# Kernel optimization log

Measured on AMD Instinct MI355X. Metric: run time of the kernel, lower is better.

## Reference

```python
import jax, jax.numpy as jnp
import numpy as np

N_NODES = 50000
N_EDGES = 500000
MUL0, MUL1 = 16, 8          # multiplicities of 0e and 1o irreps (in == out)
DIM = MUL0 + 3 * MUL1       # 40
N_BASIS, MID = 10, 32
WNUM = MUL0*MUL0 + MUL1*MUL0 + MUL0*MUL1 + MUL1*MUL1  # 576
INV_SQRT3 = 1.0 / np.sqrt(3.0)  # wigner-3j normalization for l=1 paths
FAN_IN = MUL0 + MUL1        # paths into each output irrep: 16 + 8 = 24
A0 = np.sqrt(1.0 / FAN_IN)  # sqrt((2*0+1)/fan_in)
A1 = np.sqrt(3.0 / FAN_IN)  # sqrt((2*1+1)/fan_in)
LN_EPS = 1e-5


def setup_inputs() -> dict:
    key = jax.random.key(0)
    ks = jax.random.split(key, 8)
    return {
        "x": jax.random.normal(ks[0], (N_NODES, DIM), jnp.float32),
        "edge_sh": jax.random.normal(ks[1], (N_EDGES, 4), jnp.float32),
        "edge_length_embedded": jax.random.uniform(ks[2], (N_EDGES, N_BASIS), jnp.float32),
        "W1": jax.random.normal(ks[3], (N_BASIS, MID), jnp.float32),
        "W2": jax.random.normal(ks[4], (MID, WNUM), jnp.float32),
        "gamma": jnp.ones((DIM,), jnp.float32),
        "beta": jnp.zeros((DIM,), jnp.float32),
        "edge_src": jax.random.randint(ks[5], (N_EDGES,), 0, N_NODES),
        "edge_dst": jax.random.randint(ks[6], (N_EDGES,), 0, N_NODES),
        "avg_num_neighbors": 10,
    }


def reference(x, edge_sh, edge_length_embedded, W1, W2, gamma, beta,
              edge_src, edge_dst, avg_num_neighbors):
    # radial MLP -> per-edge tensor-product weights (e3nn FullyConnectedNet style)
    h = jax.nn.silu(edge_length_embedded @ W1 / jnp.sqrt(jnp.float32(N_BASIS)))
    w = h @ W2 / jnp.sqrt(jnp.float32(MID))              # [E, 576]

    # gather node features onto edges and split into irrep blocks
    xg = x[edge_src]                                     # [E, 40]
    s = xg[:, :MUL0]                                     # [E, 16]  scalars 0e
    v = xg[:, MUL0:].reshape(-1, MUL1, 3)                # [E, 8, 3] vectors 1o
    sh0 = edge_sh[:, 0]                                  # [E]
    sh1 = edge_sh[:, 1:4]                                # [E, 3]

    # split per-edge weights by tensor-product path
    o0, o1, o2 = MUL0*MUL0, MUL0*MUL0 + MUL1*MUL0, MUL0*MUL0 + MUL1*MUL0 + MUL0*MUL1
    W_ss0 = w[:, :o0].reshape(-1, MUL0, MUL0)            # 0e x 0e -> 0e
    W_vv0 = w[:, o0:o1].reshape(-1, MUL1, MUL0)          # 1o x 1o -> 0e
    W_sv1 = w[:, o1:o2].reshape(-1, MUL0, MUL1)          # 0e x 1o -> 1o
    W_vs1 = w[:, o2:].reshape(-1, MUL1, MUL1)            # 1o x 0e -> 1o

    # weighted Clebsch-Gordan tensor product (per edge)
    vdot = jnp.einsum('eui,ei->eu', v, sh1) * INV_SQRT3  # CG 1x1->0
    out0 = A0 * (jnp.einsum('euk,eu->ek', W_ss0, s * sh0[:, None])
                 + jnp.einsum('euk,eu->ek', W_vv0, vdot))            # [E, 16]
    out1 = A1 * INV_SQRT3 * (
        jnp.einsum('euk,eu->ek', W_sv1, s)[:, :, None] * sh1[:, None, :]
        + jnp.einsum('euk,eui->eki', W_vs1, v) * sh0[:, None, None])  # [E, 8, 3]
    edge_values = jnp.concatenate([out0, out1.reshape(-1, 3 * MUL1)], axis=1)

    # scatter-sum into destination nodes, degree normalization, layernorm
    node = jax.ops.segment_sum(edge_values, edge_dst, num_segments=N_NODES)
    node = node / jnp.sqrt(jnp.float32(avg_num_neighbors))
    mu = node.mean(axis=-1, keepdims=True)
    var = node.var(axis=-1, keepdims=True)
    return (node - mu) * jax.lax.rsqrt(var + LN_EPS) * gamma + beta
```

## Files before the change

### kernel.cpp

```cpp
#include <hip/hip_runtime.h>
#include <hip/hip_bf16.h>

#define N_NODES 50000
#define N_EDGES 500000
#define MUL0 16
#define MUL1 8
#define DIM 40
#define N_BASIS 10
#define MID 32
#define WNUM 576
#define SCAN_BLOCKS 196
#define N_GROUPS (N_EDGES / 16)

typedef __attribute__((ext_vector_type(8))) short bf16x8_t;
typedef __attribute__((ext_vector_type(4))) float f32x4_t;

__device__ __forceinline__ float bf2f(unsigned short u) {
  return __uint_as_float(((unsigned int)u) << 16);
}
__device__ __forceinline__ unsigned short f2bf(float f) {
  unsigned int x = __float_as_uint(f);
  unsigned int r = x + 0x7fffu + ((x >> 16) & 1u);
  return (unsigned short)(r >> 16);
}
__device__ __forceinline__ unsigned pk2bf(float a, float b) {
  float2 f; f.x = a; f.y = b;
  __hip_bfloat162 h = __float22bfloat162_rn(f);
  return *reinterpret_cast<unsigned*>(&h);
}
__device__ __forceinline__ bool detect_bf16(const void* gamma) {
  return ((const unsigned int*)gamma)[0] == 0x3F803F80u;
}
template <bool BF16>
__device__ __forceinline__ float ld(const void* p, size_t i) {
  if (BF16) return bf2f(((const unsigned short*)p)[i]);
  return ((const float*)p)[i];
}

#define C_INV_SQRT10 0.31622776601683794f
#define C_INV_SQRT32 0.17677669529663687f
#define C_INV_SQRT3  0.5773502691896258f
#define C_A0C        0.20412414523193154f

__device__ __forceinline__ f32x4_t mfma16x16x32(bf16x8_t a, bf16x8_t b, f32x4_t c) {
  return __builtin_amdgcn_mfma_f32_16x16x32_bf16(a, b, c, 0, 0, 0);
}

__global__ __launch_bounds__(256) void rank_kernel(
    const int* __restrict__ edge_dst, int* __restrict__ cnt,
    int* __restrict__ rank) {
  int e = blockIdx.x * 256 + threadIdx.x;
  if (e < N_EDGES) rank[e] = atomicAdd(&cnt[edge_dst[e]], 1);
}

__global__ __launch_bounds__(256) void scanA_kernel(
    const int* __restrict__ cnt, int* __restrict__ off, int* __restrict__ btot) {
  __shared__ int s[256];
  const int tid = threadIdx.x;
  const int i = blockIdx.x * 256 + tid;
  int v = (i < N_NODES) ? cnt[i] : 0;
  s[tid] = v;
  __syncthreads();
  for (int d = 1; d < 256; d <<= 1) {
    int t = (tid >= d) ? s[tid - d] : 0;
    __syncthreads();
    s[tid] += t;
    __syncthreads();
  }
  if (i < N_NODES) off[i] = s[tid] - v;
  if (tid == 255) btot[blockIdx.x] = s[255];
}

__global__ __launch_bounds__(256) void scanB_kernel(
    const int* __restrict__ btot, int* __restrict__ bbase) {
  __shared__ int s[256];
  const int tid = threadIdx.x;
  int v = (tid < SCAN_BLOCKS) ? btot[tid] : 0;
  s[tid] = v;
  __syncthreads();
  for (int d = 1; d < 256; d <<= 1) {
    int t = (tid >= d) ? s[tid - d] : 0;
    __syncthreads();
    s[tid] += t;
    __syncthreads();
  }
  if (tid < SCAN_BLOCKS) bbase[tid] = s[tid] - v;
}


template <bool BF16>
__device__ void edge_mfma_body(
    const void* __restrict__ x,
    const void* __restrict__ edge_sh,
    const void* __restrict__ elemb,
    const void* __restrict__ W1,
    const void* __restrict__ W2,
    const int* __restrict__ edge_src,
    const int* __restrict__ edge_dst,
    const int* __restrict__ rank,
    const int* __restrict__ off,
    const int* __restrict__ bbase,
    unsigned short* __restrict__ ev,
    short* __restrict__ w2b, float* __restrict__ w1s, float* __restrict__ stg)
{
  const int tid = threadIdx.x;

  for (int i = tid; i < 36 * 512; i += 256) {
    int m = i / WNUM;
    int col = i - m * WNUM;
    int q = m >> 3, j = m & 7;
    int t = col >> 4, n = col & 15;
    short val;
    if (BF16) val = (short)((const unsigned short*)W2)[i];
    else      val = (short)f2bf(((const float*)W2)[i]);
    w2b[t * 512 + q * 128 + n * 8 + j] = val;
  }
  for (int i = tid; i < N_BASIS * MID; i += 256) w1s[i] = ld<BF16>(W1, i);
  __syncthreads();

  const int lane = tid & 63;
  const int wid  = tid >> 6;
  const int quad = lane >> 4;
  const int l16  = lane & 15;
  float* S = stg + wid * 832;

  for (int gi = blockIdx.x * 4 + wid; gi < N_GROUPS; gi += gridDim.x * 4) {
    const int e0 = gi * 16;
    __builtin_amdgcn_wave_barrier();

    const int eL   = e0 + l16;
    const int dL   = edge_dst[eL];
    const int posv = off[dL] + bbase[dL >> 8] + rank[eL];
    const int posA = __shfl(posv, lane >> 2, 64);
    const int posB = posv;

    if (lane < 16) {
      if (BF16) {
        uint2 sw = *reinterpret_cast<const uint2*>(
            (const unsigned short*)edge_sh + (size_t)(e0 + lane) * 4);
        S[0 * 16 + lane] = __uint_as_float(sw.x << 16);
        S[1 * 16 + lane] = __uint_as_float(sw.x & 0xffff0000u);
        S[2 * 16 + lane] = __uint_as_float(sw.y << 16);
        S[3 * 16 + lane] = __uint_as_float(sw.y & 0xffff0000u);
      } else {
        float4 s4 = *reinterpret_cast<const float4*>(
            (const float*)edge_sh + (size_t)(e0 + lane) * 4);
        S[0 * 16 + lane] = s4.x; S[1 * 16 + lane] = s4.y;
        S[2 * 16 + lane] = s4.z; S[3 * 16 + lane] = s4.w;
      }
    }

    {
      const int src = edge_src[e0 + l16];
      if (BF16) {
        const uint4* xr = reinterpret_cast<const uint4*>(
            (const unsigned short*)x + (size_t)src * DIM);
        uint4 c = xr[quad];
        unsigned wv[4] = {c.x, c.y, c.z, c.w};
        #pragma unroll
        for (int p = 0; p < 4; ++p) {
          int col = quad * 8 + 2 * p;
          float lo = __uint_as_float(wv[p] << 16);
          float hi = __uint_as_float(wv[p] & 0xffff0000u);
          int off0 = (col < 16) ? (64 + col * 16) : (448 + (col - 16) * 16);
          int off1 = (col + 1 < 16) ? (64 + (col + 1) * 16) : (448 + (col - 15) * 16);
          S[off0 + l16] = lo;
          S[off1 + l16] = hi;
        }
        if (lane < 16) {
          uint4 c4 = xr[4];
          unsigned wv4[4] = {c4.x, c4.y, c4.z, c4.w};
          #pragma unroll
          for (int p = 0; p < 4; ++p) {
            int col = 32 + 2 * p;
            S[448 + (col - 16) * 16 + lane] = __uint_as_float(wv4[p] << 16);
            S[448 + (col - 15) * 16 + lane] = __uint_as_float(wv4[p] & 0xffff0000u);
          }
        }
      } else {
        const float4* xr = reinterpret_cast<const float4*>(
            (const float*)x + (size_t)src * DIM);
        #pragma unroll
        for (int cc = 0; cc < 2; ++cc) {
          int c = quad + cc * 4;
          float4 t = xr[c];
          float vv[4] = {t.x, t.y, t.z, t.w};
          #pragma unroll
          for (int p = 0; p < 4; ++p) {
            int col = 4 * c + p;
            int offp = (col < 16) ? (64 + col * 16) : (448 + (col - 16) * 16);
            S[offp + l16] = vv[p];
          }
        }
        if (quad < 2) {
          int c = 8 + quad;
          float4 t = xr[c];
          float vv[4] = {t.x, t.y, t.z, t.w};
          #pragma unroll
          for (int p = 0; p < 4; ++p) {
            int col = 4 * c + p;
            S[448 + (col - 16) * 16 + l16] = vv[p];
          }
        }
      }
    }
    __builtin_amdgcn_wave_barrier();

    #pragma unroll
    for (int p = 0; p < 2; ++p) {
      int idx = lane + p * 64;
      int u = idx >> 4, e = idx & 15;
      float vdv = (S[448 + (u * 3 + 0) * 16 + e] * S[16 + e] +
                   S[448 + (u * 3 + 1) * 16 + e] * S[32 + e] +
                   S[448 + (u * 3 + 2) * 16 + e] * S[48 + e]) * C_INV_SQRT3;
      S[320 + u * 16 + e] = vdv;
    }
    __builtin_amdgcn_wave_barrier();

    bf16x8_t af;
    {
      float eb[N_BASIS];
      if (BF16) {
        const unsigned short* er = (const unsigned short*)elemb + (size_t)(e0 + l16) * N_BASIS;
        #pragma unroll
        for (int p = 0; p < 5; ++p) {
          unsigned uv = *reinterpret_cast<const unsigned*>(er + p * 2);
          eb[2 * p]     = __uint_as_float(uv << 16);
          eb[2 * p + 1] = __uint_as_float(uv & 0xffff0000u);
        }
      } else {
        const float* er = (const float*)elemb + (size_t)(e0 + l16) * N_BASIS;
        #pragma unroll
        for (int p = 0; p < 5; ++p) {
          float2 fv = *reinterpret_cast<const float2*>(er + p * 2);
          eb[2 * p] = fv.x; eb[2 * p + 1] = fv.y;
        }
      }
      float hv[8];
      #pragma unroll
      for (int j = 0; j < 8; ++j) {
        int k = quad * 8 + j;
        float p = 0.f;
        #pragma unroll
        for (int b = 0; b < N_BASIS; ++b) p += eb[b] * w1s[b * MID + k];
        float z = p * C_INV_SQRT10;
        hv[j] = z / (1.f + __expf(-z)) * C_INV_SQRT32;
      }
      __align__(16) unsigned au[4];
      #pragma unroll
      for (int j = 0; j < 4; ++j) au[j] = pk2bf(hv[2 * j], hv[2 * j + 1]);
      af = *reinterpret_cast<const bf16x8_t*>(au);
    }

    f32x4_t s0 = *reinterpret_cast<const f32x4_t*>(&S[quad * 4]);

    f32x4_t out0 = {0.f, 0.f, 0.f, 0.f};
    f32x4_t tsv  = {0.f, 0.f, 0.f, 0.f};
    f32x4_t tv0  = {0.f, 0.f, 0.f, 0.f};
    f32x4_t tv1  = {0.f, 0.f, 0.f, 0.f};
    f32x4_t tv2  = {0.f, 0.f, 0.f, 0.f};
    const f32x4_t zero = {0.f, 0.f, 0.f, 0.f};
    const int usel = (l16 >> 3);

    #pragma unroll
    for (int t = 0; t < 16; ++t) {
      bf16x8_t bf = *reinterpret_cast<const bf16x8_t*>(&w2b[t * 512 + lane * 8]);
      f32x4_t D = mfma16x16x32(af, bf, zero);
      f32x4_t sv = *reinterpret_cast<const f32x4_t*>(&S[64 + t * 16 + quad * 4]);
      out0 += D * (sv * s0);
    }
    #pragma unroll
    for (int t = 0; t < 8; ++t) {
      bf16x8_t bf = *reinterpret_cast<const bf16x8_t*>(&w2b[(16 + t) * 512 + lane * 8]);
      f32x4_t D = mfma16x16x32(af, bf, zero);
      f32x4_t vdv = *reinterpret_cast<const f32x4_t*>(&S[320 + t * 16 + quad * 4]);
      out0 += D * vdv;
    }
    #pragma unroll
    for (int t = 0; t < 8; ++t) {
      bf16x8_t bf = *reinterpret_cast<const bf16x8_t*>(&w2b[(24 + t) * 512 + lane * 8]);
      f32x4_t D = mfma16x16x32(af, bf, zero);
      int u = 2 * t + usel;
      f32x4_t sv = *reinterpret_cast<const f32x4_t*>(&S[64 + u * 16 + quad * 4]);
      tsv += D * sv;
    }
    #pragma unroll
    for (int t = 0; t < 4; ++t) {
      bf16x8_t bf = *reinterpret_cast<const bf16x8_t*>(&w2b[(32 + t) * 512 + lane * 8]);
      f32x4_t D = mfma16x16x32(af, bf, zero);
      int u = 2 * t + usel;
      f32x4_t v0 = *reinterpret_cast<const f32x4_t*>(&S[448 + (u * 3 + 0) * 16 + quad * 4]);
      f32x4_t v1 = *reinterpret_cast<const f32x4_t*>(&S[448 + (u * 3 + 1) * 16 + quad * 4]);
      f32x4_t v2 = *reinterpret_cast<const f32x4_t*>(&S[448 + (u * 3 + 2) * 16 + quad * 4]);
      tv0 += D * v0; tv1 += D * v1; tv2 += D * v2;
    }

    #pragma unroll
    for (int r = 0; r < 4; ++r) {
      tsv[r] += __shfl_xor(tsv[r], 8, 64);
      tv0[r] += __shfl_xor(tv0[r], 8, 64);
      tv1[r] += __shfl_xor(tv1[r], 8, 64);
      tv2[r] += __shfl_xor(tv2[r], 8, 64);
    }
    __builtin_amdgcn_wave_barrier();

    #pragma unroll
    for (int r = 0; r < 4; ++r)
      S[64 + (quad * 4 + r) * 42 + l16] = C_A0C * out0[r];
    if (l16 < 8) {
      f32x4_t h1x = *reinterpret_cast<const f32x4_t*>(&S[16 + quad * 4]);
      f32x4_t h1y = *reinterpret_cast<const f32x4_t*>(&S[32 + quad * 4]);
      f32x4_t h1z = *reinterpret_cast<const f32x4_t*>(&S[48 + quad * 4]);
      #pragma unroll
      for (int r = 0; r < 4; ++r) {
        int rowb = 64 + (quad * 4 + r) * 42 + 16 + 3 * l16;
        S[rowb + 0] = C_A0C * (tsv[r] * h1x[r] + tv0[r] * s0[r]);
        S[rowb + 1] = C_A0C * (tsv[r] * h1y[r] + tv1[r] * s0[r]);
        S[rowb + 2] = C_A0C * (tsv[r] * h1z[r] + tv2[r] * s0[r]);
      }
    }
    __builtin_amdgcn_wave_barrier();

    {
      const int edge = lane >> 2, chunk = lane & 3;
      const float* rp = &S[64 + edge * 42 + chunk * 8];
      uint4 t;
      t.x = pk2bf(rp[0], rp[1]); t.y = pk2bf(rp[2], rp[3]);
      t.z = pk2bf(rp[4], rp[5]); t.w = pk2bf(rp[6], rp[7]);
      *reinterpret_cast<uint4*>(ev + (size_t)posA * DIM + chunk * 8) = t;
      if (lane < 16) {
        const float* rq = &S[64 + lane * 42 + 32];
        uint4 t2;
        t2.x = pk2bf(rq[0], rq[1]); t2.y = pk2bf(rq[2], rq[3]);
        t2.z = pk2bf(rq[4], rq[5]); t2.w = pk2bf(rq[6], rq[7]);
        *reinterpret_cast<uint4*>(ev + (size_t)posB * DIM + 32) = t2;
      }
    }
  }
}

__global__ __launch_bounds__(256, 3) void edge_mfma_kernel(
    const void* __restrict__ x,
    const void* __restrict__ edge_sh,
    const void* __restrict__ elemb,
    const void* __restrict__ W1,
    const void* __restrict__ W2,
    const void* __restrict__ gamma,
    const int* __restrict__ edge_src,
    const int* __restrict__ edge_dst,
    const int* __restrict__ rank,
    const int* __restrict__ off,
    const int* __restrict__ bbase,
    unsigned short* __restrict__ ev)
{
  __shared__ __align__(16) short w2b[36 * 512];
  __shared__ __align__(16) float w1s[N_BASIS * MID];
  __shared__ __align__(16) float stg[4 * 832];

  if (detect_bf16(gamma))
    edge_mfma_body<true >(x, edge_sh, elemb, W1, W2, edge_src, edge_dst, rank,
                          off, bbase, ev, w2b, w1s, stg);
  else
    edge_mfma_body<false>(x, edge_sh, elemb, W1, W2, edge_src, edge_dst, rank,
                          off, bbase, ev, w2b, w1s, stg);
}


template <bool BF16>
__device__ __forceinline__ void node_body(
    const unsigned short* __restrict__ ev,
    const int* __restrict__ cnt,
    const int* __restrict__ off,
    const int* __restrict__ bbase,
    const void* __restrict__ gamma,
    const void* __restrict__ beta,
    const int* __restrict__ avg,
    void* __restrict__ out, int n, int half)
{
  const int c = cnt[n];
  const int o = off[n] + bbase[n >> 8];
  float s[20];
  #pragma unroll
  for (int d = 0; d < 20; ++d) s[d] = 0.f;

  const uint2* p = reinterpret_cast<const uint2*>(ev) + (size_t)o * 10 + half * 5;
  for (int j = 0; j < c; ++j) {
    #pragma unroll
    for (int q = 0; q < 5; ++q) {
      uint2 w = p[(size_t)j * 10 + q];
      s[q * 4 + 0] += __uint_as_float(w.x << 16);
      s[q * 4 + 1] += __uint_as_float(w.x & 0xffff0000u);
      s[q * 4 + 2] += __uint_as_float(w.y << 16);
      s[q * 4 + 3] += __uint_as_float(w.y & 0xffff0000u);
    }
  }

  const float inv = rsqrtf((float)avg[0]);
  float psum = 0.f;
  #pragma unroll
  for (int d = 0; d < 20; ++d) { s[d] *= inv; psum += s[d]; }
  const float mean = (psum + __shfl_xor(psum, 1, 64)) * (1.f / DIM);
  float pvar = 0.f;
  #pragma unroll
  for (int d = 0; d < 20; ++d) { float dd = s[d] - mean; pvar += dd * dd; }
  const float var = (pvar + __shfl_xor(pvar, 1, 64)) * (1.f / DIM);
  const float r = rsqrtf(var + 1e-5f);

  const int gb = half * 20;
  if (BF16) {
    #pragma unroll
    for (int d = 0; d < 20; ++d) {
      float y = (s[d] - mean) * r * ld<true>(gamma, gb + d) + ld<true>(beta, gb + d);
      ((unsigned short*)out)[(size_t)n * DIM + gb + d] = f2bf(y);
    }
  } else {
    float4* op = reinterpret_cast<float4*>((float*)out + (size_t)n * DIM + gb);
    #pragma unroll
    for (int q = 0; q < 5; ++q) {
      float4 t;
      t.x = (s[q*4+0] - mean) * r * ld<false>(gamma, gb+q*4+0) + ld<false>(beta, gb+q*4+0);
      t.y = (s[q*4+1] - mean) * r * ld<false>(gamma, gb+q*4+1) + ld<false>(beta, gb+q*4+1);
      t.z = (s[q*4+2] - mean) * r * ld<false>(gamma, gb+q*4+2) + ld<false>(beta, gb+q*4+2);
      t.w = (s[q*4+3] - mean) * r * ld<false>(gamma, gb+q*4+3) + ld<false>(beta, gb+q*4+3);
      op[q] = t;
    }
  }
}

__global__ __launch_bounds__(256) void node_kernel(
    const unsigned short* __restrict__ ev,
    const int* __restrict__ cnt,
    const int* __restrict__ off,
    const int* __restrict__ bbase,
    const void* __restrict__ gamma,
    const void* __restrict__ beta,
    const int* __restrict__ avg,
    void* __restrict__ out)
{
  const int t = blockIdx.x * blockDim.x + threadIdx.x;
  const int n = t >> 1;
  if (n >= N_NODES) return;
  const int half = t & 1;
  if (detect_bf16(gamma)) node_body<true >(ev, cnt, off, bbase, gamma, beta, avg, out, n, half);
  else                    node_body<false>(ev, cnt, off, bbase, gamma, beta, avg, out, n, half);
}

extern "C" void kernel_launch(void* const* d_in, const int* in_sizes, int n_in,
                              void* d_out, int out_size, void* d_ws, size_t ws_size,
                              hipStream_t stream) {
  const void* x       = d_in[0];
  const void* edge_sh = d_in[1];
  const void* elemb   = d_in[2];
  const void* W1      = d_in[3];
  const void* W2      = d_in[4];
  const void* gamma   = d_in[5];
  const void* beta    = d_in[6];
  const int* edge_src = (const int*)d_in[7];
  const int* edge_dst = (const int*)d_in[8];
  const int* avg      = (const int*)d_in[9];

  char* wsb = (char*)d_ws;
  unsigned short* ev = (unsigned short*)(wsb);
  int* rank  = (int*)(wsb + 40000000);
  int* cnt   = (int*)(wsb + 42000000);
  int* off   = (int*)(wsb + 42200000);
  int* btot  = (int*)(wsb + 42400000);
  int* bbase = (int*)(wsb + 42400800);

  hipMemsetAsync(cnt, 0, 200000, stream);

  const int EB = (N_EDGES + 255) / 256;
  rank_kernel <<<EB, 256, 0, stream>>>(edge_dst, cnt, rank);
  scanA_kernel<<<SCAN_BLOCKS, 256, 0, stream>>>(cnt, off, btot);
  scanB_kernel<<<1, 256, 0, stream>>>(btot, bbase);

  edge_mfma_kernel<<<768, 256, 0, stream>>>(x, edge_sh, elemb, W1, W2, gamma,
                                            edge_src, edge_dst, rank, off, bbase, ev);

  node_kernel<<<(2 * N_NODES + 255) / 256, 256, 0, stream>>>(
      ev, cnt, off, bbase, gamma, beta, avg, d_out);
}
```

Baseline: 216.7 us.

## Software-pipeline edge-group loads across loop iterations with register prefetch

Restructures the persistent edge loop into a software pipeline. Indices (src, dst, rank) are prefetched two groups ahead, and for the fp32 path the x rows, edge_sh, embeddings and off/bbase lookups are prefetched one group ahead into registers, so dependent gather latency overlaps with the current group's MFMA work. This costs extra VGPRs under launch_bounds(256,3), which could cause spills or lower occupancy. The bf16 path only gains the index prefetch.

```diff
diff --git a/kernel.cpp b/kernel.cpp
--- a/kernel.cpp
+++ b/kernel.cpp
@@ -124,87 +124,139 @@
   const int l16  = lane & 15;
   float* S = stg + wid * 832;
 
-  for (int gi = blockIdx.x * 4 + wid; gi < N_GROUPS; gi += gridDim.x * 4) {
+  const int stride = gridDim.x * 4;
+  int gi = blockIdx.x * 4 + wid;
+
+  int csrc, cdst, crank;
+  int coff, cbb;
+  float4 csh, cx0, cx1, cx2;
+  float  ceb[10];
+  int nsrc, ndst, nrank;
+
+  {
+    const int e = gi * 16 + l16;
+    cdst = edge_dst[e]; csrc = edge_src[e]; crank = rank[e];
+  }
+  coff = off[cdst]; cbb = bbase[cdst >> 8];
+  if constexpr (!BF16) {
+    const float4* xr = reinterpret_cast<const float4*>(
+        (const float*)x + (size_t)csrc * DIM);
+    cx0 = xr[quad]; cx1 = xr[quad + 4];
+    if (quad < 2) cx2 = xr[8 + quad];
+    if (lane < 16)
+      csh = *reinterpret_cast<const float4*>(
+          (const float*)edge_sh + (size_t)(gi * 16 + lane) * 4);
+    const float* er = (const float*)elemb + (size_t)(gi * 16 + l16) * N_BASIS;
+    #pragma unroll
+    for (int p = 0; p < 5; ++p) {
+      float2 fv = *reinterpret_cast<const float2*>(er + p * 2);
+      ceb[2 * p] = fv.x; ceb[2 * p + 1] = fv.y;
+    }
+  }
+  {
+    const int g1 = gi + stride;
+    if (g1 < N_GROUPS) {
+      const int e = g1 * 16 + l16;
+      ndst = edge_dst[e]; nsrc = edge_src[e]; nrank = rank[e];
+    } else { ndst = 0; nsrc = 0; nrank = 0; }
+  }
+
+  for (; gi < N_GROUPS; gi += stride) {
     const int e0 = gi * 16;
+    const int giN = gi + stride;
     __builtin_amdgcn_wave_barrier();
 
-    const int eL   = e0 + l16;
-    const int dL   = edge_dst[eL];
-    const int posv = off[dL] + bbase[dL >> 8] + rank[eL];
+    const int posv = coff + cbb + crank;
     const int posA = __shfl(posv, lane >> 2, 64);
     const int posB = posv;
 
-    if (lane < 16) {
-      if (BF16) {
+    if constexpr (BF16) {
+      if (lane < 16) {
         uint2 sw = *reinterpret_cast<const uint2*>(
             (const unsigned short*)edge_sh + (size_t)(e0 + lane) * 4);
         S[0 * 16 + lane] = __uint_as_float(sw.x << 16);
         S[1 * 16 + lane] = __uint_as_float(sw.x & 0xffff0000u);
         S[2 * 16 + lane] = __uint_as_float(sw.y << 16);
         S[3 * 16 + lane] = __uint_as_float(sw.y & 0xffff0000u);
-      } else {
-        float4 s4 = *reinterpret_cast<const float4*>(
-            (const float*)edge_sh + (size_t)(e0 + lane) * 4);
-        S[0 * 16 + lane] = s4.x; S[1 * 16 + lane] = s4.y;
-        S[2 * 16 + lane] = s4.z; S[3 * 16 + lane] = s4.w;
-      }
-    }
-
-    {
-      const int src = edge_src[e0 + l16];
-      if (BF16) {
-        const uint4* xr = reinterpret_cast<const uint4*>(
-            (const unsigned short*)x + (size_t)src * DIM);
-        uint4 c = xr[quad];
-        unsigned wv[4] = {c.x, c.y, c.z, c.w};
+      }
+    } else {
+      if (lane < 16) {
+        S[0 * 16 + lane] = csh.x; S[1 * 16 + lane] = csh.y;
+        S[2 * 16 + lane] = csh.z; S[3 * 16 + lane] = csh.w;
+      }
+    }
+
+    if constexpr (BF16) {
+      const int src = csrc;
+      const uint4* xr = reinterpret_cast<const uint4*>(
+          (const unsigned short*)x + (size_t)src * DIM);
+      uint4 c = xr[quad];
+      unsigned wv[4] = {c.x, c.y, c.z, c.w};
+      #pragma unroll
+      for (int p = 0; p < 4; ++p) {
+        int col = quad * 8 + 2 * p;
+        float lo = __uint_as_float(wv[p] << 16);
+        float hi = __uint_as_float(wv[p] & 0xffff0000u);
+        int off0 = (col < 16) ? (64 + col * 16) : (448 + (col - 16) * 16);
+        int off1 = (col + 1 < 16) ? (64 + (col + 1) * 16) : (448 + (col - 15) * 16);
+        S[off0 + l16] = lo;
+        S[off1 + l16] = hi;
+      }
+      if (lane < 16) {
+        uint4 c4 = xr[4];
+        unsigned wv4[4] = {c4.x, c4.y, c4.z, c4.w};
         #pragma unroll
         for (int p = 0; p < 4; ++p) {
-          int col = quad * 8 + 2 * p;
-          float lo = __uint_as_float(wv[p] << 16);
-          float hi = __uint_as_float(wv[p] & 0xffff0000u);
-          int off0 = (col < 16) ? (64 + col * 16) : (448 + (col - 16) * 16);
-          int off1 = (col + 1 < 16) ? (64 + (col + 1) * 16) : (448 + (col - 15) * 16);
-          S[off0 + l16] = lo;
-          S[off1 + l16] = hi;
+          int col = 32 + 2 * p;
+          S[448 + (col - 16) * 16 + lane] = __uint_as_float(wv4[p] << 16);
+          S[448 + (col - 15) * 16 + lane] = __uint_as_float(wv4[p] & 0xffff0000u);
         }
-        if (lane < 16) {
-          uint4 c4 = xr[4];
-          unsigned wv4[4] = {c4.x, c4.y, c4.z, c4.w};
-          #pragma unroll
-          for (int p = 0; p < 4; ++p) {
-            int col = 32 + 2 * p;
-            S[448 + (col - 16) * 16 + lane] = __uint_as_float(wv4[p] << 16);
-            S[448 + (col - 15) * 16 + lane] = __uint_as_float(wv4[p] & 0xffff0000u);
-          }
+      }
+    } else {
+      float v0[4] = {cx0.x, cx0.y, cx0.z, cx0.w};
+      #pragma unroll
+      for (int p = 0; p < 4; ++p)
+        S[64 + (4 * quad + p) * 16 + l16] = v0[p];
+      float v1[4] = {cx1.x, cx1.y, cx1.z, cx1.w};
+      #pragma unroll
+      for (int p = 0; p < 4; ++p)
+        S[448 + (4 * quad + p) * 16 + l16] = v1[p];
+      if (quad < 2) {
+        float v2[4] = {cx2.x, cx2.y, cx2.z, cx2.w};
+        #pragma unroll
+        for (int p = 0; p < 4; ++p)
+          S[448 + (16 + 4 * quad + p) * 16 + l16] = v2[p];
+      }
+    }
+    __builtin_amdgcn_wave_barrier();
+
+    float4 zsh, zx0, zx1, zx2;
+    float  zeb[10];
+    int zoff = 0, zbb = 0;
+    int msrc = 0, mdst = 0, mrank = 0;
+    if (giN < N_GROUPS) {
+      zoff = off[ndst]; zbb = bbase[ndst >> 8];
+      if constexpr (!BF16) {
+        const float4* xr = reinterpret_cast<const float4*>(
+            (const float*)x + (size_t)nsrc * DIM);
+        zx0 = xr[quad]; zx1 = xr[quad + 4];
+        if (quad < 2) zx2 = xr[8 + quad];
+        if (lane < 16)
+          zsh = *reinterpret_cast<const float4*>(
+              (const float*)edge_sh + (size_t)(giN * 16 + lane) * 4);
+        const float* er = (const float*)elemb + (size_t)(giN * 16 + l16) * N_BASIS;
+        #pragma unroll
+        for (int p = 0; p < 5; ++p) {
+          float2 fv = *reinterpret_cast<const float2*>(er + p * 2);
+          zeb[2 * p] = fv.x; zeb[2 * p + 1] = fv.y;
         }
-      } else {
-        const float4* xr = reinterpret_cast<const float4*>(
-            (const float*)x + (size_t)src * DIM);
-        #pragma unroll
-        for (int cc = 0; cc < 2; ++cc) {
-          int c = quad + cc * 4;
-          float4 t = xr[c];
-          float vv[4] = {t.x, t.y, t.z, t.w};
-          #pragma unroll
-          for (int p = 0; p < 4; ++p) {
-            int col = 4 * c + p;
-            int offp = (col < 16) ? (64 + col * 16) : (448 + (col - 16) * 16);
-            S[offp + l16] = vv[p];
-          }
-        }
-        if (quad < 2) {
-          int c = 8 + quad;
-          float4 t = xr[c];
-          float vv[4] = {t.x, t.y, t.z, t.w};
-          #pragma unroll
-          for (int p = 0; p < 4; ++p) {
-            int col = 4 * c + p;
-            S[448 + (col - 16) * 16 + l16] = vv[p];
-          }
-        }
-      }
-    }
-    __builtin_amdgcn_wave_barrier();
+      }
+      const int gi2 = giN + stride;
+      if (gi2 < N_GROUPS) {
+        const int e = gi2 * 16 + l16;
+        mdst = edge_dst[e]; msrc = edge_src[e]; mrank = rank[e];
+      }
+    }
 
     #pragma unroll
     for (int p = 0; p < 2; ++p) {
@@ -220,7 +272,7 @@
     bf16x8_t af;
     {
       float eb[N_BASIS];
-      if (BF16) {
+      if constexpr (BF16) {
         const unsigned short* er = (const unsigned short*)elemb + (size_t)(e0 + l16) * N_BASIS;
         #pragma unroll
         for (int p = 0; p < 5; ++p) {
@@ -229,12 +281,8 @@
           eb[2 * p + 1] = __uint_as_float(uv & 0xffff0000u);
         }
       } else {
-        const float* er = (const float*)elemb + (size_t)(e0 + l16) * N_BASIS;
         #pragma unroll
-        for (int p = 0; p < 5; ++p) {
-          float2 fv = *reinterpret_cast<const float2*>(er + p * 2);
-          eb[2 * p] = fv.x; eb[2 * p + 1] = fv.y;
-        }
+        for (int b = 0; b < N_BASIS; ++b) eb[b] = ceb[b];
       }
       float hv[8];
       #pragma unroll
@@ -336,6 +384,15 @@
         *reinterpret_cast<uint4*>(ev + (size_t)posB * DIM + 32) = t2;
       }
     }
+
+    csrc = nsrc; cdst = ndst; crank = nrank;
+    coff = zoff; cbb = zbb;
+    if constexpr (!BF16) {
+      csh = zsh; cx0 = zx0; cx1 = zx1; cx2 = zx2;
+      #pragma unroll
+      for (int b = 0; b < 10; ++b) ceb[b] = zeb[b];
+    }
+    nsrc = msrc; ndst = mdst; nrank = mrank;
   }
 }
 
```

After: 269.6 us. 1.24x slower.

## Double-buffer edge gathers via async global-to-LDS loads and fold scan base into offsets

Applied to the files above, without the earlier changes.

For the fp32 path, the edge kernel now prefetches the next group's gathered node features and spherical harmonics straight into a second LDS staging buffer with global_load_lds. Explicit vmcnt waits let that gather overlap the current group's MFMA work, and the index loads are software-pipelined two groups ahead. The block-base scan results are now added into the offsets by a multi-block scanB, which removes the extra bbase lookup from the edge and node kernels. The cost is doubled LDS staging, with occupancy lowered to 2 blocks per CU and a grid of 512.

```diff
diff --git a/kernel.cpp b/kernel.cpp
--- a/kernel.cpp
+++ b/kernel.cpp
@@ -44,6 +44,12 @@
 
 __device__ __forceinline__ f32x4_t mfma16x16x32(bf16x8_t a, bf16x8_t b, f32x4_t c) {
   return __builtin_amdgcn_mfma_f32_16x16x32_bf16(a, b, c, 0, 0, 0);
+}
+
+__device__ __forceinline__ void gload4(const float* g, float* l) {
+  __builtin_amdgcn_global_load_lds(
+      (const __attribute__((address_space(1))) void*)g,
+      (__attribute__((address_space(3))) void*)l, 4, 0, 0);
 }
 
 __global__ __launch_bounds__(256) void rank_kernel(
@@ -72,8 +78,9 @@
 }
 
 __global__ __launch_bounds__(256) void scanB_kernel(
-    const int* __restrict__ btot, int* __restrict__ bbase) {
+    const int* __restrict__ btot, int* __restrict__ off) {
   __shared__ int s[256];
+  __shared__ int basev;
   const int tid = threadIdx.x;
   int v = (tid < SCAN_BLOCKS) ? btot[tid] : 0;
   s[tid] = v;
@@ -84,9 +91,28 @@
     s[tid] += t;
     __syncthreads();
   }
-  if (tid < SCAN_BLOCKS) bbase[tid] = s[tid] - v;
-}
-
+  if (tid == 0) basev = (blockIdx.x == 0) ? 0 : s[blockIdx.x - 1];
+  __syncthreads();
+  const int i = blockIdx.x * 256 + tid;
+  if (i < N_NODES) off[i] += basev;
+}
+
+
+#define STAGE_OPS 11
+
+__device__ __forceinline__ void stage_issue(float* Sn, int g, int psrc,
+                                            const float* xf, const float* shf,
+                                            int lane) {
+  const int quad = lane >> 4;
+  const int l16  = lane & 15;
+  gload4(shf + ((size_t)g * 16 + l16) * 4 + quad, Sn);
+  const float* gx = xf + (size_t)psrc * DIM + quad;
+  #pragma unroll
+  for (int i = 0; i < 10; ++i) {
+    float* lb = (i < 4) ? (Sn + 64 + 64 * i) : (Sn + 192 + 64 * i);
+    gload4(gx + i * 4, lb);
+  }
+}
 
 template <bool BF16>
 __device__ void edge_mfma_body(
@@ -99,7 +125,6 @@
     const int* __restrict__ edge_dst,
     const int* __restrict__ rank,
     const int* __restrict__ off,
-    const int* __restrict__ bbase,
     unsigned short* __restrict__ ev,
     short* __restrict__ w2b, float* __restrict__ w1s, float* __restrict__ stg)
 {
@@ -122,37 +147,28 @@
   const int wid  = tid >> 6;
   const int quad = lane >> 4;
   const int l16  = lane & 15;
-  float* S = stg + wid * 832;
-
-  for (int gi = blockIdx.x * 4 + wid; gi < N_GROUPS; gi += gridDim.x * 4) {
-    const int e0 = gi * 16;
-    __builtin_amdgcn_wave_barrier();
-
-    const int eL   = e0 + l16;
-    const int dL   = edge_dst[eL];
-    const int posv = off[dL] + bbase[dL >> 8] + rank[eL];
-    const int posA = __shfl(posv, lane >> 2, 64);
-    const int posB = posv;
-
-    if (lane < 16) {
-      if (BF16) {
+  float* Sw = stg + wid * 1664;
+
+  if constexpr (BF16) {
+    float* S = Sw;
+    for (int gi = blockIdx.x * 4 + wid; gi < N_GROUPS; gi += gridDim.x * 4) {
+      const int e0 = gi * 16;
+      __builtin_amdgcn_wave_barrier();
+      const int eL   = e0 + l16;
+      const int dL   = edge_dst[eL];
+      const int posv = off[dL] + rank[eL];
+      const int posA = __shfl(posv, lane >> 2, 64);
+      const int posB = posv;
+      if (lane < 16) {
         uint2 sw = *reinterpret_cast<const uint2*>(
             (const unsigned short*)edge_sh + (size_t)(e0 + lane) * 4);
         S[0 * 16 + lane] = __uint_as_float(sw.x << 16);
         S[1 * 16 + lane] = __uint_as_float(sw.x & 0xffff0000u);
         S[2 * 16 + lane] = __uint_as_float(sw.y << 16);
         S[3 * 16 + lane] = __uint_as_float(sw.y & 0xffff0000u);
-      } else {
-        float4 s4 = *reinterpret_cast<const float4*>(
-            (const float*)edge_sh + (size_t)(e0 + lane) * 4);
-        S[0 * 16 + lane] = s4.x; S[1 * 16 + lane] = s4.y;
-        S[2 * 16 + lane] = s4.z; S[3 * 16 + lane] = s4.w;
-      }
-    }
-
-    {
-      const int src = edge_src[e0 + l16];
-      if (BF16) {
+      }
+      {
+        const int src = edge_src[e0 + l16];
         const uint4* xr = reinterpret_cast<const uint4*>(
             (const unsigned short*)x + (size_t)src * DIM);
         uint4 c = xr[quad];
@@ -177,34 +193,171 @@
             S[448 + (col - 15) * 16 + lane] = __uint_as_float(wv4[p] & 0xffff0000u);
           }
         }
-      } else {
-        const float4* xr = reinterpret_cast<const float4*>(
-            (const float*)x + (size_t)src * DIM);
+      }
+      __builtin_amdgcn_wave_barrier();
+      #pragma unroll
+      for (int p = 0; p < 2; ++p) {
+        int idx = lane + p * 64;
+        int u = idx >> 4, e = idx & 15;
+        float vdv = (S[448 + (u * 3 + 0) * 16 + e] * S[16 + e] +
+                     S[448 + (u * 3 + 1) * 16 + e] * S[32 + e] +
+                     S[448 + (u * 3 + 2) * 16 + e] * S[48 + e]) * C_INV_SQRT3;
+        S[320 + u * 16 + e] = vdv;
+      }
+      __builtin_amdgcn_wave_barrier();
+      bf16x8_t af;
+      {
+        float eb[N_BASIS];
+        const unsigned short* er = (const unsigned short*)elemb + (size_t)(e0 + l16) * N_BASIS;
         #pragma unroll
-        for (int cc = 0; cc < 2; ++cc) {
-          int c = quad + cc * 4;
-          float4 t = xr[c];
-          float vv[4] = {t.x, t.y, t.z, t.w};
+        for (int p = 0; p < 5; ++p) {
+          unsigned uv = *reinterpret_cast<const unsigned*>(er + p * 2);
+          eb[2 * p]     = __uint_as_float(uv << 16);
+          eb[2 * p + 1] = __uint_as_float(uv & 0xffff0000u);
+        }
+        float hv[8];
+        #pragma unroll
+        for (int j = 0; j < 8; ++j) {
+          int k = quad * 8 + j;
+          float p = 0.f;
           #pragma unroll
-          for (int p = 0; p < 4; ++p) {
-            int col = 4 * c + p;
-            int offp = (col < 16) ? (64 + col * 16) : (448 + (col - 16) * 16);
-            S[offp + l16] = vv[p];
-          }
+          for (int b = 0; b < N_BASIS; ++b) p += eb[b] * w1s[b * MID + k];
+          float z = p * C_INV_SQRT10;
+          hv[j] = z / (1.f + __expf(-z)) * C_INV_SQRT32;
         }
-        if (quad < 2) {
-          int c = 8 + quad;
-          float4 t = xr[c];
-          float vv[4] = {t.x, t.y, t.z, t.w};
-          #pragma unroll
-          for (int p = 0; p < 4; ++p) {
-            int col = 4 * c + p;
-            S[448 + (col - 16) * 16 + l16] = vv[p];
-          }
+        __align__(16) unsigned au[4];
+        #pragma unroll
+        for (int j = 0; j < 4; ++j) au[j] = pk2bf(hv[2 * j], hv[2 * j + 1]);
+        af = *reinterpret_cast<const bf16x8_t*>(au);
+      }
+      f32x4_t s0 = *reinterpret_cast<const f32x4_t*>(&S[quad * 4]);
+      f32x4_t out0 = {0.f,0.f,0.f,0.f}, tsv = {0.f,0.f,0.f,0.f};
+      f32x4_t tv0 = {0.f,0.f,0.f,0.f}, tv1 = {0.f,0.f,0.f,0.f}, tv2 = {0.f,0.f,0.f,0.f};
+      const f32x4_t zero = {0.f,0.f,0.f,0.f};
+      const int usel = (l16 >> 3);
+      #pragma unroll
+      for (int t = 0; t < 16; ++t) {
+        bf16x8_t bf = *reinterpret_cast<const bf16x8_t*>(&w2b[t * 512 + lane * 8]);
+        f32x4_t D = mfma16x16x32(af, bf, zero);
+        f32x4_t sv = *reinterpret_cast<const f32x4_t*>(&S[64 + t * 16 + quad * 4]);
+        out0 += D * (sv * s0);
+      }
+      #pragma unroll
+      for (int t = 0; t < 8; ++t) {
+        bf16x8_t bf = *reinterpret_cast<const bf16x8_t*>(&w2b[(16 + t) * 512 + lane * 8]);
+        f32x4_t D = mfma16x16x32(af, bf, zero);
+        f32x4_t vdv = *reinterpret_cast<const f32x4_t*>(&S[320 + t * 16 + quad * 4]);
+        out0 += D * vdv;
+      }
+      #pragma unroll
+      for (int t = 0; t < 8; ++t) {
+        bf16x8_t bf = *reinterpret_cast<const bf16x8_t*>(&w2b[(24 + t) * 512 + lane * 8]);
+        f32x4_t D = mfma16x16x32(af, bf, zero);
+        int u = 2 * t + usel;
+        f32x4_t sv = *reinterpret_cast<const f32x4_t*>(&S[64 + u * 16 + quad * 4]);
+        tsv += D * sv;
+      }
+      #pragma unroll
+      for (int t = 0; t < 4; ++t) {
+        bf16x8_t bf = *reinterpret_cast<const bf16x8_t*>(&w2b[(32 + t) * 512 + lane * 8]);
+        f32x4_t D = mfma16x16x32(af, bf, zero);
+        int u = 2 * t + usel;
+        f32x4_t v0 = *reinterpret_cast<const f32x4_t*>(&S[448 + (u * 3 + 0) * 16 + quad * 4]);
+        f32x4_t v1 = *reinterpret_cast<const f32x4_t*>(&S[448 + (u * 3 + 1) * 16 + quad * 4]);
+        f32x4_t v2 = *reinterpret_cast<const f32x4_t*>(&S[448 + (u * 3 + 2) * 16 + quad * 4]);
+        tv0 += D * v0; tv1 += D * v1; tv2 += D * v2;
+      }
+      #pragma unroll
+      for (int r = 0; r < 4; ++r) {
+        tsv[r] += __shfl_xor(tsv[r], 8, 64);
+        tv0[r] += __shfl_xor(tv0[r], 8, 64);
+        tv1[r] += __shfl_xor(tv1[r], 8, 64);
+        tv2[r] += __shfl_xor(tv2[r], 8, 64);
+      }
+      __builtin_amdgcn_wave_barrier();
+      #pragma unroll
+      for (int r = 0; r < 4; ++r)
+        S[64 + (quad * 4 + r) * 42 + l16] = C_A0C * out0[r];
+      if (l16 < 8) {
+        f32x4_t h1x = *reinterpret_cast<const f32x4_t*>(&S[16 + quad * 4]);
+        f32x4_t h1y = *reinterpret_cast<const f32x4_t*>(&S[32 + quad * 4]);
+        f32x4_t h1z = *reinterpret_cast<const f32x4_t*>(&S[48 + quad * 4]);
+        #pragma unroll
+        for (int r = 0; r < 4; ++r) {
+          int rowb = 64 + (quad * 4 + r) * 42 + 16 + 3 * l16;
+          S[rowb + 0] = C_A0C * (tsv[r] * h1x[r] + tv0[r] * s0[r]);
+          S[rowb + 1] = C_A0C * (tsv[r] * h1y[r] + tv1[r] * s0[r]);
+          S[rowb + 2] = C_A0C * (tsv[r] * h1z[r] + tv2[r] * s0[r]);
         }
       }
-    }
+      __builtin_amdgcn_wave_barrier();
+      {
+        const int edge = lane >> 2, chunk = lane & 3;
+        const float* rp = &S[64 + edge * 42 + chunk * 8];
+        uint4 t;
+        t.x = pk2bf(rp[0], rp[1]); t.y = pk2bf(rp[2], rp[3]);
+        t.z = pk2bf(rp[4], rp[5]); t.w = pk2bf(rp[6], rp[7]);
+        *reinterpret_cast<uint4*>(ev + (size_t)posA * DIM + chunk * 8) = t;
+        if (lane < 16) {
+          const float* rq = &S[64 + lane * 42 + 32];
+          uint4 t2;
+          t2.x = pk2bf(rq[0], rq[1]); t2.y = pk2bf(rq[2], rq[3]);
+          t2.z = pk2bf(rq[4], rq[5]); t2.w = pk2bf(rq[6], rq[7]);
+          *reinterpret_cast<uint4*>(ev + (size_t)posB * DIM + 32) = t2;
+        }
+      }
+    }
+    return;
+  }
+
+  const float* xf  = (const float*)x;
+  const float* shf = (const float*)edge_sh;
+  const int stride = gridDim.x * 4;
+  const int gi0 = blockIdx.x * 4 + wid;
+
+  int pdst, psrc, prank;
+  int cdst, crank;
+  {
+    const int e = gi0 * 16 + l16;
+    pdst = edge_dst[e]; psrc = edge_src[e]; prank = rank[e];
+  }
+  stage_issue(Sw, gi0, psrc, xf, shf, lane);
+  cdst = pdst; crank = prank;
+  {
+    const int g1 = gi0 + stride;
+    if (g1 < N_GROUPS) {
+      const int e = g1 * 16 + l16;
+      pdst = edge_dst[e]; psrc = edge_src[e]; prank = rank[e];
+    }
+  }
+
+  int cur = 0;
+  for (int gi = gi0; gi < N_GROUPS; gi += stride, cur ^= 1) {
+    float* S  = Sw + cur * 832;
+    float* Sn = Sw + (cur ^ 1) * 832;
+    const int e0 = gi * 16;
+    const int g1 = gi + stride;
+
     __builtin_amdgcn_wave_barrier();
+    if (g1 < N_GROUPS) {
+      stage_issue(Sn, g1, psrc, xf, shf, lane);
+      asm volatile("s_waitcnt vmcnt(11)" ::: "memory");
+    } else {
+      asm volatile("s_waitcnt vmcnt(0)" ::: "memory");
+    }
+    __builtin_amdgcn_sched_barrier(0);
+
+    const int ndst = pdst, nrank = prank;
+    {
+      const int g2 = g1 + stride;
+      if (g2 < N_GROUPS) {
+        const int e = g2 * 16 + l16;
+        pdst = edge_dst[e]; psrc = edge_src[e]; prank = rank[e];
+      }
+    }
+    const int posv = off[cdst] + crank;
+    const int posA = __shfl(posv, lane >> 2, 64);
+    const int posB = posv;
 
     #pragma unroll
     for (int p = 0; p < 2; ++p) {
@@ -220,21 +373,11 @@
     bf16x8_t af;
     {
       float eb[N_BASIS];
-      if (BF16) {
-        const unsigned short* er = (const unsigned short*)elemb + (size_t)(e0 + l16) * N_BASIS;
-        #pragma unroll
-        for (int p = 0; p < 5; ++p) {
-          unsigned uv = *reinterpret_cast<const unsigned*>(er + p * 2);
-          eb[2 * p]     = __uint_as_float(uv << 16);
-          eb[2 * p + 1] = __uint_as_float(uv & 0xffff0000u);
-        }
-      } else {
-        const float* er = (const float*)elemb + (size_t)(e0 + l16) * N_BASIS;
-        #pragma unroll
-        for (int p = 0; p < 5; ++p) {
-          float2 fv = *reinterpret_cast<const float2*>(er + p * 2);
-          eb[2 * p] = fv.x; eb[2 * p + 1] = fv.y;
-        }
+      const float* er = (const float*)elemb + (size_t)(e0 + l16) * N_BASIS;
+      #pragma unroll
+      for (int p = 0; p < 5; ++p) {
+        float2 fv = *reinterpret_cast<const float2*>(er + p * 2);
+        eb[2 * p] = fv.x; eb[2 * p + 1] = fv.y;
       }
       float hv[8];
       #pragma unroll
@@ -336,10 +479,12 @@
         *reinterpret_cast<uint4*>(ev + (size_t)posB * DIM + 32) = t2;
       }
     }
-  }
-}
-
-__global__ __launch_bounds__(256, 3) void edge_mfma_kernel(
+
+    cdst = ndst; crank = nrank;
+  }
+}
+
+__global__ __launch_bounds__(256, 2) void edge_mfma_kernel(
     const void* __restrict__ x,
     const void* __restrict__ edge_sh,
     const void* __restrict__ elemb,
@@ -350,19 +495,18 @@
     const int* __restrict__ edge_dst,
     const int* __restrict__ rank,
     const int* __restrict__ off,
-    const int* __restrict__ bbase,
     unsigned short* __restrict__ ev)
 {
   __shared__ __align__(16) short w2b[36 * 512];
   __shared__ __align__(16) float w1s[N_BASIS * MID];
-  __shared__ __align__(16) float stg[4 * 832];
+  __shared__ __align__(16) float stg[4 * 1664];
 
   if (detect_bf16(gamma))
     edge_mfma_body<true >(x, edge_sh, elemb, W1, W2, edge_src, edge_dst, rank,
-                          off, bbase, ev, w2b, w1s, stg);
+                          off, ev, w2b, w1s, stg);
   else
     edge_mfma_body<false>(x, edge_sh, elemb, W1, W2, edge_src, edge_dst, rank,
-                          off, bbase, ev, w2b, w1s, stg);
+                          off, ev, w2b, w1s, stg);
 }
 
 
@@ -371,14 +515,13 @@
     const unsigned short* __restrict__ ev,
     const int* __restrict__ cnt,
     const int* __restrict__ off,
-    const int* __restrict__ bbase,
     const void* __restrict__ gamma,
     const void* __restrict__ beta,
     const int* __restrict__ avg,
     void* __restrict__ out, int n, int half)
 {
   const int c = cnt[n];
-  const int o = off[n] + bbase[n >> 8];
+  const int o = off[n];
   float s[20];
   #pragma unroll
   for (int d = 0; d < 20; ++d) s[d] = 0.f;
@@ -431,7 +574,6 @@
     const unsigned short* __restrict__ ev,
     const int* __restrict__ cnt,
     const int* __restrict__ off,
-    const int* __restrict__ bbase,
     const void* __restrict__ gamma,
     const void* __restrict__ beta,
     const int* __restrict__ avg,
@@ -441,8 +583,8 @@
   const int n = t >> 1;
   if (n >= N_NODES) return;
   const int half = t & 1;
-  if (detect_bf16(gamma)) node_body<true >(ev, cnt, off, bbase, gamma, beta, avg, out, n, half);
-  else                    node_body<false>(ev, cnt, off, bbase, gamma, beta, avg, out, n, half);
+  if (detect_bf16(gamma)) node_body<true >(ev, cnt, off, gamma, beta, avg, out, n, half);
+  else                    node_body<false>(ev, cnt, off, gamma, beta, avg, out, n, half);
 }
 
 extern "C" void kernel_launch(void* const* d_in, const int* in_sizes, int n_in,
@@ -465,18 +607,17 @@
   int* cnt   = (int*)(wsb + 42000000);
   int* off   = (int*)(wsb + 42200000);
   int* btot  = (int*)(wsb + 42400000);
-  int* bbase = (int*)(wsb + 42400800);
 
   hipMemsetAsync(cnt, 0, 200000, stream);
 
   const int EB = (N_EDGES + 255) / 256;
   rank_kernel <<<EB, 256, 0, stream>>>(edge_dst, cnt, rank);
   scanA_kernel<<<SCAN_BLOCKS, 256, 0, stream>>>(cnt, off, btot);
-  scanB_kernel<<<1, 256, 0, stream>>>(btot, bbase);
-
-  edge_mfma_kernel<<<768, 256, 0, stream>>>(x, edge_sh, elemb, W1, W2, gamma,
-                                            edge_src, edge_dst, rank, off, bbase, ev);
+  scanB_kernel<<<SCAN_BLOCKS, 256, 0, stream>>>(btot, off);
+
+  edge_mfma_kernel<<<512, 256, 0, stream>>>(x, edge_sh, elemb, W1, W2, gamma,
+                                            edge_src, edge_dst, rank, off, ev);
 
   node_kernel<<<(2 * N_NODES + 255) / 256, 256, 0, stream>>>(
-      ev, cnt, off, bbase, gamma, beta, avg, d_out);
-}
+      ev, cnt, off, gamma, beta, avg, d_out);
+}
```

New measurement: 216.7 us. Within noise of the previous version (-0.0%).
